# Optimization experiments

Measured on AMD Instinct MI355X. Metric: run time of the kernel, lower is better.

Reference implementation:

```python
import jax, jax.numpy as jnp
import numpy as np
import math

NUM_HEADS = 8


def _dwconv(x, w, b, pad):
    # depthwise conv: x (B,C,H,W), w (C,1,k,k)
    c = x.shape[1]
    y = jax.lax.conv_general_dilated(
        x, w, window_strides=(1, 1), padding=[(pad, pad), (pad, pad)],
        feature_group_count=c, dimension_numbers=("NCHW", "OIHW", "NCHW"))
    return y + b[None, :, None, None]


def _conv(x, w, b, pad):
    y = jax.lax.conv_general_dilated(
        x, w, window_strides=(1, 1), padding=[(pad, pad), (pad, pad)],
        dimension_numbers=("NCHW", "OIHW", "NCHW"))
    return y + b[None, :, None, None]


def setup_inputs() -> dict:
    key = jax.random.key(0)
    ks = jax.random.split(key, 6)
    B, C, H, W = 8, 128, 128, 128
    x = jax.random.normal(ks[0], (B, C, H, W), dtype=jnp.float32)
    wq = jax.random.normal(ks[1], (C, 1, 9, 9), dtype=jnp.float32) * 0.05
    wk = jax.random.normal(ks[2], (C, 1, 9, 9), dtype=jnp.float32) * 0.05
    wv = jax.random.normal(ks[3], (C, 1, 9, 9), dtype=jnp.float32) * 0.05
    wo = jax.random.normal(ks[4], (C, C, 3, 3), dtype=jnp.float32) * 0.02
    bq = jnp.zeros((C,), jnp.float32)
    bk = jnp.zeros((C,), jnp.float32)
    bv = jnp.zeros((C,), jnp.float32)
    bo = jnp.zeros((C,), jnp.float32)
    return {"x": x, "wq": wq, "bq": bq, "wk": wk, "bk": bk,
            "wv": wv, "bv": bv, "wo": wo, "bo": bo}


def reference(x, wq, bq, wk, bk, wv, bv, wo, bo):
    b, c, h, w = x.shape
    hds = NUM_HEADS
    d = (h * w) // hds  # spatial dim split across heads
    q = _dwconv(x, wq, bq, 4).reshape(b, c, hds, d).transpose(0, 2, 1, 3)  # (b,hds,c,d)
    k = _dwconv(x, wk, bk, 4).reshape(b, c, hds, d).transpose(0, 2, 3, 1)  # (b,hds,d,c)
    v = _dwconv(x, wv, bv, 4).reshape(b, c, hds, d).transpose(0, 2, 1, 3)  # (b,hds,c,d)
    # channel attention: C x C scores per head, fp32 softmax
    qk = jnp.einsum("bhcd,bhde->bhce", q.astype(jnp.float32), k.astype(jnp.float32)) / math.sqrt(h * w)
    a = jnp.einsum("bhce,bhed->bhcd", jax.nn.softmax(qk, axis=-1), v.astype(jnp.float32))
    a = a.transpose(0, 2, 1, 3).reshape(b, c, h, w)
    return _conv(a, wo, bo, 1)
```

## Files before the change

kernel.cpp:

```cpp
#include <hip/hip_runtime.h>

#define BATCH 8
#define CH 128
#define HH 128
#define WW 128
#define HWSZ 16384
#define NHEADS 8
#define DHEAD 2048

typedef short bf16x8 __attribute__((ext_vector_type(8)));
typedef short bf16x4v __attribute__((ext_vector_type(4)));
typedef float f32x4 __attribute__((ext_vector_type(4)));
typedef float f32x2 __attribute__((ext_vector_type(2)));
typedef _Float16 f16x8 __attribute__((ext_vector_type(8)));
typedef _Float16 f16x4 __attribute__((ext_vector_type(4)));

static __device__ inline unsigned short f2bf(float f) {
    unsigned u = __builtin_bit_cast(unsigned, f);
    u += 0x7fff + ((u >> 16) & 1);
    return (unsigned short)(u >> 16);
}

__global__ __launch_bounds__(256) void toeplitz_prep_kernel(
    const float* __restrict__ wq, const float* __restrict__ wk,
    const float* __restrict__ wv, _Float16* __restrict__ Tp)
{
    const int g = blockIdx.x * 256 + threadIdx.x;
    const int c    = g / 1728;
    const int rem  = g - c * 1728;
    const int m    = rem >> 6;
    const int lane = rem & 63;
    const int conv = m / 9;
    const int dy   = m - conv * 9;
    const float* w = (conv == 0) ? wq : ((conv == 1) ? wk : wv);
    const int j    = lane & 15;
    const int kb   = (lane >> 4) << 3;
    f16x8 h;
    #pragma unroll
    for (int e = 0; e < 8; ++e) {
        const int d = kb + e - j;
        h[e] = (d >= 0 && d <= 8) ? (_Float16)w[c * 81 + dy * 9 + d]
                                  : (_Float16)0.f;
    }
    *(f16x8*)&Tp[(size_t)g * 8] = h;
}

__global__ __launch_bounds__(256) void dwconv_qkv_mfma_kernel(
    const float* __restrict__ x,
    const float* __restrict__ bq, const float* __restrict__ bk,
    const float* __restrict__ bv,
    const _Float16* __restrict__ Tp,
    unsigned short* __restrict__ Qb, unsigned short* __restrict__ Kb,
    unsigned short* __restrict__ Vb)
{
    const int bc = blockIdx.x;
    const int b  = bc >> 7;
    const int c  = bc & (CH - 1);

    __shared__ _Float16 img[136][144];

    const int tid  = threadIdx.x;
    const int wave = tid >> 6;
    const int lane = tid & 63;
    const int lx   = lane & 15;
    const int qd   = lane >> 4;

    f16x8 Btp[27];
    const _Float16* tp = Tp + (size_t)c * 13824 + (size_t)lane * 8;
    #pragma unroll
    for (int m = 0; m < 27; ++m)
        Btp[m] = *(const f16x8*)(tp + (size_t)m * 512);

    {
        f16x8 z = {0, 0, 0, 0, 0, 0, 0, 0};
        _Float16* flat = &img[0][0];
        for (int i = tid; i < 2448; i += 256)
            *(f16x8*)&flat[i * 8] = z;
    }
    __syncthreads();
    const float* xp = x + (size_t)bc * HWSZ;
    for (int i = tid; i < 4096; i += 256) {
        const float4 v = *(const float4*)&xp[i * 4];
        const int y  = i >> 5;
        const int xc = (i & 31) << 2;
        f16x4 h = {(_Float16)v.x, (_Float16)v.y, (_Float16)v.z, (_Float16)v.w};
        *(f16x4*)&img[y + 4][xc + 4] = h;
    }
    __syncthreads();

    const float bqv = bq[c], bkv = bk[c], bvv = bv[c];

    #pragma unroll 1
    for (int t = 0; t < 8; ++t) {
        const int sg = t * 4 + wave;
        const int yg = sg >> 2;
        const int y0 = yg << 4;
        const int x0 = (sg & 3) << 5;

        f32x4 aq0 = {bqv, bqv, bqv, bqv}, aq1 = aq0;
        f32x4 ak0 = {bkv, bkv, bkv, bkv}, ak1 = ak0;
        f32x4 av0 = {bvv, bvv, bvv, bvv}, av1 = av0;

        const _Float16* rp = &img[y0 + lx][x0 + (qd << 3)];
        #pragma unroll
        for (int dy = 0; dy < 9; ++dy) {
            const f16x8 a0 = *(const f16x8*)rp;
            const f16x8 a1 = *(const f16x8*)(rp + 16);
            rp += 144;
            aq0 = __builtin_amdgcn_mfma_f32_16x16x32_f16(Btp[dy],      a0, aq0, 0, 0, 0);
            aq1 = __builtin_amdgcn_mfma_f32_16x16x32_f16(Btp[dy],      a1, aq1, 0, 0, 0);
            ak0 = __builtin_amdgcn_mfma_f32_16x16x32_f16(Btp[9 + dy],  a0, ak0, 0, 0, 0);
            ak1 = __builtin_amdgcn_mfma_f32_16x16x32_f16(Btp[9 + dy],  a1, ak1, 0, 0, 0);
            av0 = __builtin_amdgcn_mfma_f32_16x16x32_f16(Btp[18 + dy], a0, av0, 0, 0, 0);
            av1 = __builtin_amdgcn_mfma_f32_16x16x32_f16(Btp[18 + dy], a1, av1, 0, 0, 0);
        }

        const size_t base = ((size_t)(b * 8 + yg) * CH + c) * DHEAD
                          + (size_t)lx * WW + x0 + (qd << 2);
        bf16x4v h;
        h[0] = (short)f2bf(aq0[0]); h[1] = (short)f2bf(aq0[1]);
        h[2] = (short)f2bf(aq0[2]); h[3] = (short)f2bf(aq0[3]);
        *(bf16x4v*)&Qb[base] = h;
        h[0] = (short)f2bf(aq1[0]); h[1] = (short)f2bf(aq1[1]);
        h[2] = (short)f2bf(aq1[2]); h[3] = (short)f2bf(aq1[3]);
        *(bf16x4v*)&Qb[base + 16] = h;
        h[0] = (short)f2bf(ak0[0]); h[1] = (short)f2bf(ak0[1]);
        h[2] = (short)f2bf(ak0[2]); h[3] = (short)f2bf(ak0[3]);
        *(bf16x4v*)&Kb[base] = h;
        h[0] = (short)f2bf(ak1[0]); h[1] = (short)f2bf(ak1[1]);
        h[2] = (short)f2bf(ak1[2]); h[3] = (short)f2bf(ak1[3]);
        *(bf16x4v*)&Kb[base + 16] = h;
        h[0] = (short)f2bf(av0[0]); h[1] = (short)f2bf(av0[1]);
        h[2] = (short)f2bf(av0[2]); h[3] = (short)f2bf(av0[3]);
        *(bf16x4v*)&Vb[base] = h;
        h[0] = (short)f2bf(av1[0]); h[1] = (short)f2bf(av1[1]);
        h[2] = (short)f2bf(av1[2]); h[3] = (short)f2bf(av1[3]);
        *(bf16x4v*)&Vb[base + 16] = h;
    }
}

__global__ __launch_bounds__(256) void qks_kernel(
    const unsigned short* __restrict__ Qb, const unsigned short* __restrict__ Kb,
    unsigned short* __restrict__ Pb)
{
    const int blk = ((blockIdx.x & 7) << 5) | (blockIdx.x >> 3);
    const int bh  = blk >> 2;
    const int c0  = (blk & 3) << 5;

    __shared__ __align__(16) char smem[41216];

    const int tid  = threadIdx.x;
    const int wave = tid >> 6;
    const int lane = tid & 63;
    const int lx   = lane & 15;
    const int qd   = lane >> 4;
    const int n0   = wave << 5;

    f32x4 acc[2][2];
    #pragma unroll
    for (int mi = 0; mi < 2; ++mi)
        #pragma unroll
        for (int ni = 0; ni < 2; ++ni) acc[mi][ni] = (f32x4){0.f, 0.f, 0.f, 0.f};

    const unsigned short* Qp = Qb + ((size_t)bh * CH + c0) * DHEAD;
    const unsigned short* Kp = Kb + (size_t)bh * CH * DHEAD;

    #pragma unroll 1
    for (int chk = 0; chk < 16; ++chk) {
        const int t0 = chk << 7;
        __syncthreads();
        for (int i = tid; i < 512; i += 256) {
            const int r = i >> 4, u = i & 15;
            const bf16x8 v = *(const bf16x8*)&Qp[(size_t)r * DHEAD + t0 + u * 8];
            const unsigned off = (unsigned)((r << 8) + (u << 4)) ^ (((unsigned)r & 7u) << 4);
            *(bf16x8*)(smem + off) = v;
        }
        for (int i = tid; i < 2048; i += 256) {
            const int r = i >> 4, u = i & 15;
            const bf16x8 v = *(const bf16x8*)&Kp[(size_t)r * DHEAD + t0 + u * 8];
            const unsigned off = 8192u + ((unsigned)((r << 8) + (u << 4)) ^ (((unsigned)r & 7u) << 4));
            *(bf16x8*)(smem + off) = v;
        }
        __syncthreads();
        #pragma unroll
        for (int ki = 0; ki < 4; ++ki) {
            const int kc = ki * 32 + qd * 8;
            bf16x8 a[2], bv[2];
            #pragma unroll
            for (int mi = 0; mi < 2; ++mi) {
                const int r = mi * 16 + lx;
                a[mi] = *(const bf16x8*)(smem +
                        ((unsigned)((r << 8) + (kc << 1)) ^ (((unsigned)r & 7u) << 4)));
            }
            #pragma unroll
            for (int ni = 0; ni < 2; ++ni) {
                const int r = n0 + ni * 16 + lx;
                bv[ni] = *(const bf16x8*)(smem + 8192u +
                        ((unsigned)((r << 8) + (kc << 1)) ^ (((unsigned)r & 7u) << 4)));
            }
            #pragma unroll
            for (int mi = 0; mi < 2; ++mi)
                #pragma unroll
                for (int ni = 0; ni < 2; ++ni)
                    acc[mi][ni] = __builtin_amdgcn_mfma_f32_16x16x32_bf16(
                        a[mi], bv[ni], acc[mi][ni], 0, 0, 0);
        }
    }

    __syncthreads();
    float* Ss = (float*)smem;
    #pragma unroll
    for (int mi = 0; mi < 2; ++mi)
        #pragma unroll
        for (int ni = 0; ni < 2; ++ni)
            #pragma unroll
            for (int r = 0; r < 4; ++r)
                Ss[(mi * 16 + qd * 4 + r) * 132 + n0 + ni * 16 + lx] = acc[mi][ni][r];
    __syncthreads();

    const int rr   = tid >> 3;
    const int col0 = (tid & 7) << 4;
    f32x4 v0 = *(const f32x4*)&Ss[rr * 132 + col0];
    f32x4 v1 = *(const f32x4*)&Ss[rr * 132 + col0 + 4];
    f32x4 v2 = *(const f32x4*)&Ss[rr * 132 + col0 + 8];
    f32x4 v3 = *(const f32x4*)&Ss[rr * 132 + col0 + 12];
    const f32x4 sc = {0.0078125f, 0.0078125f, 0.0078125f, 0.0078125f};
    v0 *= sc; v1 *= sc; v2 *= sc; v3 *= sc;
    float m = v0[0];
    #pragma unroll
    for (int j = 1; j < 4; ++j) m = fmaxf(m, v0[j]);
    #pragma unroll
    for (int j = 0; j < 4; ++j) { m = fmaxf(m, v1[j]); m = fmaxf(m, v2[j]); m = fmaxf(m, v3[j]); }
    m = fmaxf(m, __shfl_xor(m, 1));
    m = fmaxf(m, __shfl_xor(m, 2));
    m = fmaxf(m, __shfl_xor(m, 4));
    float e[16];
    #pragma unroll
    for (int j = 0; j < 4; ++j) {
        e[j]      = __expf(v0[j] - m);
        e[4 + j]  = __expf(v1[j] - m);
        e[8 + j]  = __expf(v2[j] - m);
        e[12 + j] = __expf(v3[j] - m);
    }
    float s = 0.f;
    #pragma unroll
    for (int j = 0; j < 16; ++j) s += e[j];
    s += __shfl_xor(s, 1);
    s += __shfl_xor(s, 2);
    s += __shfl_xor(s, 4);
    const float inv = 1.f / s;
    bf16x8 h0, h1;
    #pragma unroll
    for (int j = 0; j < 8; ++j) {
        h0[j] = (short)f2bf(e[j] * inv);
        h1[j] = (short)f2bf(e[8 + j] * inv);
    }
    unsigned short* prow = Pb + ((size_t)bh * CH + c0 + rr) * CH + col0;
    *(bf16x8*)&prow[0] = h0;
    *(bf16x8*)&prow[8] = h1;
}

__global__ __launch_bounds__(256) void pv_mfma_kernel(
    const unsigned short* __restrict__ Pb, const unsigned short* __restrict__ Vb,
    unsigned short* __restrict__ At)
{
    const int blk = blockIdx.x;
    const int t0  = (blk & 15) << 7;
    const int bh  = blk >> 4;

    __shared__ __align__(16) char smem[69632];
    unsigned short (*Ps)[136] = (unsigned short(*)[136])smem;
    unsigned short (*Vs)[136] = (unsigned short(*)[136])(smem + 34816);
    float (*So)[132] = (float(*)[132])smem;

    const int tid  = threadIdx.x;
    const int wave = tid >> 6;
    const int lane = tid & 63;
    const int lx   = lane & 15;
    const int qd   = lane >> 4;
    const int m0   = (wave & 1) * 64;
    const int n0   = (wave >> 1) * 64;

    const unsigned short* Pp = Pb + (size_t)bh * CH * CH;
    const unsigned short* Vp = Vb + (size_t)bh * CH * DHEAD;

    for (int i = tid; i < 2048; i += 256) {
        const int r  = i >> 4;
        const int cl = (i & 15) << 3;
        *(bf16x8*)&Ps[r][cl] = *(const bf16x8*)&Pp[(size_t)r * CH + cl];
    }
    for (int i = tid; i < 2048; i += 256) {
        const int e   = i & 127;
        const int tc8 = (i >> 7) << 3;
        const bf16x8 vv = *(const bf16x8*)&Vp[(size_t)e * DHEAD + t0 + tc8];
        #pragma unroll
        for (int j = 0; j < 8; ++j) Vs[tc8 + j][e] = (unsigned short)vv[j];
    }
    __syncthreads();

    f32x4 acc[4][4];
    #pragma unroll
    for (int mi = 0; mi < 4; ++mi)
        #pragma unroll
        for (int ni = 0; ni < 4; ++ni) acc[mi][ni] = (f32x4){0.f, 0.f, 0.f, 0.f};

    #pragma unroll
    for (int ki = 0; ki < 4; ++ki) {
        const int kc = ki * 32 + qd * 8;
        bf16x8 a[4], bv[4];
        #pragma unroll
        for (int mi = 0; mi < 4; ++mi)
            a[mi] = *(const bf16x8*)&Ps[m0 + mi * 16 + lx][kc];
        #pragma unroll
        for (int ni = 0; ni < 4; ++ni)
            bv[ni] = *(const bf16x8*)&Vs[n0 + ni * 16 + lx][kc];
        #pragma unroll
        for (int mi = 0; mi < 4; ++mi)
            #pragma unroll
            for (int ni = 0; ni < 4; ++ni)
                acc[mi][ni] = __builtin_amdgcn_mfma_f32_16x16x32_bf16(
                    a[mi], bv[ni], acc[mi][ni], 0, 0, 0);
    }

    __syncthreads();
    #pragma unroll
    for (int mi = 0; mi < 4; ++mi)
        #pragma unroll
        for (int ni = 0; ni < 4; ++ni)
            #pragma unroll
            for (int r = 0; r < 4; ++r)
                So[n0 + ni * 16 + lx][m0 + mi * 16 + qd * 4 + r] = acc[mi][ni][r];
    __syncthreads();

    const int t  = tid >> 1;
    const int ch = (tid & 1) * 64;
    const size_t orow = (((size_t)(bh >> 3) * HWSZ) + (size_t)(bh & 7) * DHEAD + t0 + t) * CH + ch;
    #pragma unroll
    for (int j = 0; j < 8; ++j) {
        const float4 f0 = *(const float4*)&So[t][ch + j * 8];
        const float4 f1 = *(const float4*)&So[t][ch + j * 8 + 4];
        bf16x8 h;
        h[0] = (short)f2bf(f0.x); h[1] = (short)f2bf(f0.y);
        h[2] = (short)f2bf(f0.z); h[3] = (short)f2bf(f0.w);
        h[4] = (short)f2bf(f1.x); h[5] = (short)f2bf(f1.y);
        h[6] = (short)f2bf(f1.z); h[7] = (short)f2bf(f1.w);
        *(bf16x8*)&At[orow + j * 8] = h;
    }
}

__global__ __launch_bounds__(256) void wprep_kernel(
    const float* __restrict__ wo, unsigned short* __restrict__ Wt)
{
    const int i = blockIdx.x * 256 + threadIdx.x;
    const int tap = i >> 14;
    const int rem = i & 16383;
    const int co  = rem >> 7;
    const int ci  = rem & 127;
    Wt[i] = f2bf(wo[(size_t)(co * CH + ci) * 9 + tap]);
}

__global__ __launch_bounds__(512, 2) void conv3x3_mfma_kernel(
    const unsigned short* __restrict__ At, const unsigned short* __restrict__ Wt,
    const float* __restrict__ bo, float* __restrict__ out)
{
    __shared__ __align__(16) char smem[163840];

    const int w    = ((blockIdx.x & 7) << 6) | (blockIdx.x >> 3);
    const int yp   = w & 63;
    const int b    = w >> 6;
    const int y0   = yp << 1;

    const int tid  = threadIdx.x;
    const int wave = tid >> 6;
    const int lane = tid & 63;
    const int lx   = lane & 15;
    const int qd   = lane >> 4;
    const int m0   = (wave & 1) << 6;
    const int n0   = (wave >> 1) << 6;
    const int rsel = n0 >> 7;
    const int xb   = n0 & 64;

    const int j0 = tid, j1 = tid + 512;
    const int co0 = j0 >> 3, cu0 = j0 & 7;
    const int co1 = j1 >> 3, cu1 = j1 & 7;
    const unsigned swo0 = (unsigned)((co0 * 128 + cu0 * 16) ^ ((co0 & 7) << 4)) + 131072u;
    const unsigned swo1 = (unsigned)((co1 * 128 + cu1 * 16) ^ ((co1 & 7) << 4)) + 131072u;

    float4 nwa = *(const float4*)&Wt[(size_t)co0 * 128 + cu0 * 8];
    float4 nwb = *(const float4*)&Wt[(size_t)co1 * 128 + cu1 * 8];

    const size_t abase = (size_t)b * HWSZ * CH;
    for (int i = tid; i < 8192; i += 512) {
        const int r   = i >> 11;
        const int rem = i & 2047;
        const int xx  = rem >> 4;
        const int u   = rem & 15;
        const int gy  = y0 - 1 + r;
        float4 v = make_float4(0.f, 0.f, 0.f, 0.f);
        if ((unsigned)gy < HH)
            v = *(const float4*)&At[abase + (size_t)gy * WW * CH + xx * CH + u * 8];
        const int xp = xx + 1;
        const unsigned off = (unsigned)((r << 15) + (xx << 8) + (u << 4))
                           ^ (((unsigned)xp & 7u) << 4);
        *(float4*)(smem + off) = v;
    }
    *(float4*)(smem + swo0) = nwa;
    *(float4*)(smem + swo1) = nwb;
    nwa = *(const float4*)&Wt[(size_t)co0 * 128 + 64 + cu0 * 8];
    nwb = *(const float4*)&Wt[(size_t)co1 * 128 + 64 + cu1 * 8];

    f32x4 acc[4][4];
    #pragma unroll
    for (int mi = 0; mi < 4; ++mi) {
        f32x4 bv;
        #pragma unroll
        for (int r = 0; r < 4; ++r) bv[r] = bo[m0 + mi * 16 + qd * 4 + r];
        #pragma unroll
        for (int ni = 0; ni < 4; ++ni) acc[mi][ni] = bv;
    }

    __syncthreads();

    #pragma unroll 1
    for (int s = 0; s < 18; ++s) {
        const int tap = s >> 1;
        const int dy  = (tap * 11) >> 5;
        const int txc = tap - dy * 3;
        const int kh  = s & 1;
        const int ra  = rsel + dy;
        const unsigned wbase = 131072u + (unsigned)(s & 1) * 16384u;

        #pragma unroll
        for (int ks = 0; ks < 2; ++ks) {
            const int wkb = ks * 64 + qd * 16;
            const int akb = kh * 128 + ks * 64 + qd * 16;
            bf16x8 a[4], bfr[4];
            #pragma unroll
            for (int mi = 0; mi < 4; ++mi) {
                const int co = m0 + mi * 16 + lx;
                a[mi] = *(const bf16x8*)(smem + wbase +
                        (unsigned)((co * 128 + wkb) ^ ((co & 7) << 4)));
            }
            #pragma unroll
            for (int ni = 0; ni < 4; ++ni) {
                const int xp = xb + ni * 16 + lx + txc;
                const bool z = (unsigned)(xp - 1) >= 128u;
                const int xpc = z ? 1 : xp;
                const unsigned off = (unsigned)((ra << 15) + ((xpc - 1) << 8) + akb)
                                   ^ (((unsigned)xpc & 7u) << 4);
                bfr[ni] = *(const bf16x8*)(smem + off);
                if (z) bfr[ni] = (bf16x8){0, 0, 0, 0, 0, 0, 0, 0};
            }
            #pragma unroll
            for (int mi = 0; mi < 4; ++mi)
                #pragma unroll
                for (int ni = 0; ni < 4; ++ni)
                    acc[mi][ni] = __builtin_amdgcn_mfma_f32_16x16x32_bf16(
                        a[mi], bfr[ni], acc[mi][ni], 0, 0, 0);
        }
        if (s < 17) {
            const unsigned nb = 131072u + (unsigned)((s + 1) & 1) * 16384u;
            *(float4*)(smem + (swo0 - 131072u) + nb) = nwa;
            *(float4*)(smem + (swo1 - 131072u) + nb) = nwb;
            if (s < 16) {
                const int s2 = s + 2;
                const size_t gb = (size_t)(s2 >> 1) * 16384 + (s2 & 1) * 64;
                nwa = *(const float4*)&Wt[gb + co0 * 128 + cu0 * 8];
                nwb = *(const float4*)&Wt[gb + co1 * 128 + cu1 * 8];
            }
        }
        __syncthreads();
    }

    const int gy = y0 + rsel;
    const size_t obase = (size_t)b * CH * HWSZ + (size_t)gy * WW + xb;
    #pragma unroll
    for (int mi = 0; mi < 4; ++mi) {
        #pragma unroll
        for (int r = 0; r < 4; ++r) {
            const int co = m0 + mi * 16 + qd * 4 + r;
            float* orow = out + obase + (size_t)co * HWSZ;
            #pragma unroll
            for (int ni = 0; ni < 4; ++ni)
                orow[ni * 16 + lx] = acc[mi][ni][r];
        }
    }
}

extern "C" void kernel_launch(void* const* d_in, const int* in_sizes, int n_in,
                              void* d_out, int out_size, void* d_ws, size_t ws_size,
                              hipStream_t stream)
{
    const float* x  = (const float*)d_in[0];
    const float* wq = (const float*)d_in[1];
    const float* bq = (const float*)d_in[2];
    const float* wk = (const float*)d_in[3];
    const float* bk = (const float*)d_in[4];
    const float* wv = (const float*)d_in[5];
    const float* bv = (const float*)d_in[6];
    const float* wo = (const float*)d_in[7];
    const float* bo = (const float*)d_in[8];

    char* ws = (char*)d_ws;
    unsigned short* Qb    = (unsigned short*)(ws);
    unsigned short* Kb    = (unsigned short*)(ws + (size_t)33554432);
    unsigned short* Vb    = (unsigned short*)(ws + (size_t)67108864);
    unsigned short* Pb    = (unsigned short*)(ws + (size_t)134217728);
    unsigned short* At    = (unsigned short*)(ws + (size_t)136314880);
    unsigned short* Wt    = (unsigned short*)(ws + (size_t)169869312);
    _Float16*       Tp    = (_Float16*)      (ws + (size_t)100663296);

    toeplitz_prep_kernel<<<864, 256, 0, stream>>>(wq, wk, wv, Tp);
    dwconv_qkv_mfma_kernel<<<BATCH * CH, 256, 0, stream>>>(x, bq, bk, bv, Tp, Qb, Kb, Vb);
    wprep_kernel<<<576, 256, 0, stream>>>(wo, Wt);
    qks_kernel<<<256, 256, 0, stream>>>(Qb, Kb, Pb);
    pv_mfma_kernel<<<64 * 16, 256, 0, stream>>>(Pb, Vb, At);
    conv3x3_mfma_kernel<<<BATCH * 64, 512, 0, stream>>>(At, Wt, bo, (float*)d_out);
}
```

Measured before the change: 291.1 us.

## Split QK-softmax into 16-row tiles over 512 blocks and transpose dwconv MFMA outputs

The QK^T softmax kernel now gives each block 16 query channels instead of 32, doubling the grid to 512 blocks to improve occupancy and CU coverage. The cost is that every K chunk is loaded from global memory twice as often. Separately, the depthwise-conv MFMA operands are swapped so the accumulator layout is transposed, and outputs are written as scalar 2-byte stores instead of 4-wide vector stores. The scalar stores may coalesce worse.

```diff
diff --git a/kernel.cpp b/kernel.cpp
--- a/kernel.cpp
+++ b/kernel.cpp
@@ -107,35 +107,25 @@
             const f16x8 a0 = *(const f16x8*)rp;
             const f16x8 a1 = *(const f16x8*)(rp + 16);
             rp += 144;
-            aq0 = __builtin_amdgcn_mfma_f32_16x16x32_f16(Btp[dy],      a0, aq0, 0, 0, 0);
-            aq1 = __builtin_amdgcn_mfma_f32_16x16x32_f16(Btp[dy],      a1, aq1, 0, 0, 0);
-            ak0 = __builtin_amdgcn_mfma_f32_16x16x32_f16(Btp[9 + dy],  a0, ak0, 0, 0, 0);
-            ak1 = __builtin_amdgcn_mfma_f32_16x16x32_f16(Btp[9 + dy],  a1, ak1, 0, 0, 0);
-            av0 = __builtin_amdgcn_mfma_f32_16x16x32_f16(Btp[18 + dy], a0, av0, 0, 0, 0);
-            av1 = __builtin_amdgcn_mfma_f32_16x16x32_f16(Btp[18 + dy], a1, av1, 0, 0, 0);
+            aq0 = __builtin_amdgcn_mfma_f32_16x16x32_f16(a0, Btp[dy],      aq0, 0, 0, 0);
+            aq1 = __builtin_amdgcn_mfma_f32_16x16x32_f16(a1, Btp[dy],      aq1, 0, 0, 0);
+            ak0 = __builtin_amdgcn_mfma_f32_16x16x32_f16(a0, Btp[9 + dy],  ak0, 0, 0, 0);
+            ak1 = __builtin_amdgcn_mfma_f32_16x16x32_f16(a1, Btp[9 + dy],  ak1, 0, 0, 0);
+            av0 = __builtin_amdgcn_mfma_f32_16x16x32_f16(a0, Btp[18 + dy], av0, 0, 0, 0);
+            av1 = __builtin_amdgcn_mfma_f32_16x16x32_f16(a1, Btp[18 + dy], av1, 0, 0, 0);
         }
 
         const size_t base = ((size_t)(b * 8 + yg) * CH + c) * DHEAD
-                          + (size_t)lx * WW + x0 + (qd << 2);
-        bf16x4v h;
-        h[0] = (short)f2bf(aq0[0]); h[1] = (short)f2bf(aq0[1]);
-        h[2] = (short)f2bf(aq0[2]); h[3] = (short)f2bf(aq0[3]);
-        *(bf16x4v*)&Qb[base] = h;
-        h[0] = (short)f2bf(aq1[0]); h[1] = (short)f2bf(aq1[1]);
-        h[2] = (short)f2bf(aq1[2]); h[3] = (short)f2bf(aq1[3]);
-        *(bf16x4v*)&Qb[base + 16] = h;
-        h[0] = (short)f2bf(ak0[0]); h[1] = (short)f2bf(ak0[1]);
-        h[2] = (short)f2bf(ak0[2]); h[3] = (short)f2bf(ak0[3]);
-        *(bf16x4v*)&Kb[base] = h;
-        h[0] = (short)f2bf(ak1[0]); h[1] = (short)f2bf(ak1[1]);
-        h[2] = (short)f2bf(ak1[2]); h[3] = (short)f2bf(ak1[3]);
-        *(bf16x4v*)&Kb[base + 16] = h;
-        h[0] = (short)f2bf(av0[0]); h[1] = (short)f2bf(av0[1]);
-        h[2] = (short)f2bf(av0[2]); h[3] = (short)f2bf(av0[3]);
-        *(bf16x4v*)&Vb[base] = h;
-        h[0] = (short)f2bf(av1[0]); h[1] = (short)f2bf(av1[1]);
-        h[2] = (short)f2bf(av1[2]); h[3] = (short)f2bf(av1[3]);
-        *(bf16x4v*)&Vb[base + 16] = h;
+                          + (size_t)(qd << 2) * WW + x0 + lx;
+        #pragma unroll
+        for (int r = 0; r < 4; ++r) {
+            Qb[base + r * WW]      = f2bf(aq0[r]);
+            Qb[base + r * WW + 16] = f2bf(aq1[r]);
+            Kb[base + r * WW]      = f2bf(ak0[r]);
+            Kb[base + r * WW + 16] = f2bf(ak1[r]);
+            Vb[base + r * WW]      = f2bf(av0[r]);
+            Vb[base + r * WW + 16] = f2bf(av1[r]);
+        }
     }
 }
 
@@ -143,11 +133,11 @@
     const unsigned short* __restrict__ Qb, const unsigned short* __restrict__ Kb,
     unsigned short* __restrict__ Pb)
 {
-    const int blk = ((blockIdx.x & 7) << 5) | (blockIdx.x >> 3);
-    const int bh  = blk >> 2;
-    const int c0  = (blk & 3) << 5;
-
-    __shared__ __align__(16) char smem[41216];
+    const int o    = blockIdx.x;
+    const int bh   = o & 63;
+    const int c0   = (o >> 6) << 4;
+
+    __shared__ __align__(16) char smem[36864];
 
     const int tid  = threadIdx.x;
     const int wave = tid >> 6;
@@ -156,108 +146,84 @@
     const int qd   = lane >> 4;
     const int n0   = wave << 5;
 
-    f32x4 acc[2][2];
-    #pragma unroll
-    for (int mi = 0; mi < 2; ++mi)
-        #pragma unroll
-        for (int ni = 0; ni < 2; ++ni) acc[mi][ni] = (f32x4){0.f, 0.f, 0.f, 0.f};
+    f32x4 acc0 = {0.f, 0.f, 0.f, 0.f}, acc1 = acc0;
 
     const unsigned short* Qp = Qb + ((size_t)bh * CH + c0) * DHEAD;
     const unsigned short* Kp = Kb + (size_t)bh * CH * DHEAD;
+
+    const int qr = tid >> 4, qu = tid & 15;
+    const unsigned qoff = (unsigned)((qr << 8) + (qu << 4)) ^ (((unsigned)qr & 7u) << 4);
 
     #pragma unroll 1
     for (int chk = 0; chk < 16; ++chk) {
         const int t0 = chk << 7;
         __syncthreads();
-        for (int i = tid; i < 512; i += 256) {
-            const int r = i >> 4, u = i & 15;
-            const bf16x8 v = *(const bf16x8*)&Qp[(size_t)r * DHEAD + t0 + u * 8];
-            const unsigned off = (unsigned)((r << 8) + (u << 4)) ^ (((unsigned)r & 7u) << 4);
-            *(bf16x8*)(smem + off) = v;
+        {
+            const bf16x8 v = *(const bf16x8*)&Qp[(size_t)qr * DHEAD + t0 + qu * 8];
+            *(bf16x8*)(smem + qoff) = v;
         }
         for (int i = tid; i < 2048; i += 256) {
             const int r = i >> 4, u = i & 15;
             const bf16x8 v = *(const bf16x8*)&Kp[(size_t)r * DHEAD + t0 + u * 8];
-            const unsigned off = 8192u + ((unsigned)((r << 8) + (u << 4)) ^ (((unsigned)r & 7u) << 4));
+            const unsigned off = 4096u +
+                ((unsigned)((r << 8) + (u << 4)) ^ (((unsigned)r & 7u) << 4));
             *(bf16x8*)(smem + off) = v;
         }
         __syncthreads();
         #pragma unroll
         for (int ki = 0; ki < 4; ++ki) {
-            const int kc = ki * 32 + qd * 8;
-            bf16x8 a[2], bv[2];
-            #pragma unroll
-            for (int mi = 0; mi < 2; ++mi) {
-                const int r = mi * 16 + lx;
-                a[mi] = *(const bf16x8*)(smem +
-                        ((unsigned)((r << 8) + (kc << 1)) ^ (((unsigned)r & 7u) << 4)));
-            }
-            #pragma unroll
-            for (int ni = 0; ni < 2; ++ni) {
-                const int r = n0 + ni * 16 + lx;
-                bv[ni] = *(const bf16x8*)(smem + 8192u +
-                        ((unsigned)((r << 8) + (kc << 1)) ^ (((unsigned)r & 7u) << 4)));
-            }
-            #pragma unroll
-            for (int mi = 0; mi < 2; ++mi)
-                #pragma unroll
-                for (int ni = 0; ni < 2; ++ni)
-                    acc[mi][ni] = __builtin_amdgcn_mfma_f32_16x16x32_bf16(
-                        a[mi], bv[ni], acc[mi][ni], 0, 0, 0);
+            const int kcb = (ki * 32 + qd * 8) << 1;
+            const bf16x8 a = *(const bf16x8*)(smem +
+                ((unsigned)((lx << 8) + kcb) ^ (((unsigned)lx & 7u) << 4)));
+            const int r0 = n0 + lx, r1 = n0 + 16 + lx;
+            const bf16x8 b0 = *(const bf16x8*)(smem + 4096u +
+                ((unsigned)((r0 << 8) + kcb) ^ (((unsigned)r0 & 7u) << 4)));
+            const bf16x8 b1 = *(const bf16x8*)(smem + 4096u +
+                ((unsigned)((r1 << 8) + kcb) ^ (((unsigned)r1 & 7u) << 4)));
+            acc0 = __builtin_amdgcn_mfma_f32_16x16x32_bf16(a, b0, acc0, 0, 0, 0);
+            acc1 = __builtin_amdgcn_mfma_f32_16x16x32_bf16(a, b1, acc1, 0, 0, 0);
         }
     }
 
     __syncthreads();
     float* Ss = (float*)smem;
     #pragma unroll
-    for (int mi = 0; mi < 2; ++mi)
-        #pragma unroll
-        for (int ni = 0; ni < 2; ++ni)
-            #pragma unroll
-            for (int r = 0; r < 4; ++r)
-                Ss[(mi * 16 + qd * 4 + r) * 132 + n0 + ni * 16 + lx] = acc[mi][ni][r];
-    __syncthreads();
-
-    const int rr   = tid >> 3;
-    const int col0 = (tid & 7) << 4;
-    f32x4 v0 = *(const f32x4*)&Ss[rr * 132 + col0];
-    f32x4 v1 = *(const f32x4*)&Ss[rr * 132 + col0 + 4];
-    f32x4 v2 = *(const f32x4*)&Ss[rr * 132 + col0 + 8];
-    f32x4 v3 = *(const f32x4*)&Ss[rr * 132 + col0 + 12];
+    for (int r = 0; r < 4; ++r) {
+        Ss[(qd * 4 + r) * 132 + n0 + lx]      = acc0[r];
+        Ss[(qd * 4 + r) * 132 + n0 + 16 + lx] = acc1[r];
+    }
+    __syncthreads();
+
+    const int rr = tid >> 4;
+    const int c8 = (tid & 15) << 3;
+    f32x4 v0 = *(const f32x4*)&Ss[rr * 132 + c8];
+    f32x4 v1 = *(const f32x4*)&Ss[rr * 132 + c8 + 4];
     const f32x4 sc = {0.0078125f, 0.0078125f, 0.0078125f, 0.0078125f};
-    v0 *= sc; v1 *= sc; v2 *= sc; v3 *= sc;
-    float m = v0[0];
-    #pragma unroll
-    for (int j = 1; j < 4; ++j) m = fmaxf(m, v0[j]);
-    #pragma unroll
-    for (int j = 0; j < 4; ++j) { m = fmaxf(m, v1[j]); m = fmaxf(m, v2[j]); m = fmaxf(m, v3[j]); }
+    v0 *= sc; v1 *= sc;
+    float m = fmaxf(fmaxf(fmaxf(v0[0], v0[1]), fmaxf(v0[2], v0[3])),
+                    fmaxf(fmaxf(v1[0], v1[1]), fmaxf(v1[2], v1[3])));
     m = fmaxf(m, __shfl_xor(m, 1));
     m = fmaxf(m, __shfl_xor(m, 2));
     m = fmaxf(m, __shfl_xor(m, 4));
-    float e[16];
+    m = fmaxf(m, __shfl_xor(m, 8));
+    float e[8];
     #pragma unroll
     for (int j = 0; j < 4; ++j) {
-        e[j]      = __expf(v0[j] - m);
-        e[4 + j]  = __expf(v1[j] - m);
-        e[8 + j]  = __expf(v2[j] - m);
-        e[12 + j] = __expf(v3[j] - m);
+        e[j]     = __expf(v0[j] - m);
+        e[4 + j] = __expf(v1[j] - m);
     }
     float s = 0.f;
     #pragma unroll
-    for (int j = 0; j < 16; ++j) s += e[j];
+    for (int j = 0; j < 8; ++j) s += e[j];
     s += __shfl_xor(s, 1);
     s += __shfl_xor(s, 2);
     s += __shfl_xor(s, 4);
+    s += __shfl_xor(s, 8);
     const float inv = 1.f / s;
-    bf16x8 h0, h1;
-    #pragma unroll
-    for (int j = 0; j < 8; ++j) {
-        h0[j] = (short)f2bf(e[j] * inv);
-        h1[j] = (short)f2bf(e[8 + j] * inv);
-    }
-    unsigned short* prow = Pb + ((size_t)bh * CH + c0 + rr) * CH + col0;
-    *(bf16x8*)&prow[0] = h0;
-    *(bf16x8*)&prow[8] = h1;
+    bf16x8 h;
+    #pragma unroll
+    for (int j = 0; j < 8; ++j) h[j] = (short)f2bf(e[j] * inv);
+    *(bf16x8*)&Pb[((size_t)bh * CH + c0 + rr) * CH + c8] = h;
 }
 
 __global__ __launch_bounds__(256) void pv_mfma_kernel(
@@ -513,7 +479,7 @@
     toeplitz_prep_kernel<<<864, 256, 0, stream>>>(wq, wk, wv, Tp);
     dwconv_qkv_mfma_kernel<<<BATCH * CH, 256, 0, stream>>>(x, bq, bk, bv, Tp, Qb, Kb, Vb);
     wprep_kernel<<<576, 256, 0, stream>>>(wo, Wt);
-    qks_kernel<<<256, 256, 0, stream>>>(Qb, Kb, Pb);
+    qks_kernel<<<512, 256, 0, stream>>>(Qb, Kb, Pb);
     pv_mfma_kernel<<<64 * 16, 256, 0, stream>>>(Pb, Vb, At);
     conv3x3_mfma_kernel<<<BATCH * 64, 512, 0, stream>>>(At, Wt, bo, (float*)d_out);
 }
```

Result: faster. 277.6 us (-4.6%).
